# Kernel tuning notes

Hardware: AMD Instinct MI355X
Metric: run time of the kernel (lower is better)

Reference implementation:

```python
import jax, jax.numpy as jnp
import numpy as np

B, S, D, H, DH = 4, 2048, 512, 8, 64

def setup_inputs() -> dict:
    key = jax.random.key(0)
    k1, k2, k3, k4 = jax.random.split(key, 4)
    sc = 1.0 / np.sqrt(D)
    return {
        "x": jax.random.normal(k1, (B, S, D), dtype=jnp.float32),
        "Wq": jax.random.normal(k2, (H, D, DH), dtype=jnp.float32) * sc,
        "Wk": jax.random.normal(k3, (H, D, DH), dtype=jnp.float32) * sc,
        "Wv": jax.random.normal(k4, (H, D, DH), dtype=jnp.float32) * sc,
    }

def reference(x, Wq, Wk, Wv):
    # x: [B,S,D]; Wq/Wk/Wv: [H,D,DH] (stacked per-head bias-free Linear weights)
    q = jnp.einsum('bsd,hdk->bhsk', x, Wq)
    k = jnp.einsum('bsd,hdk->bhsk', x, Wk)
    v = jnp.einsum('bsd,hdk->bhsk', x, Wv)
    scale = DH ** -0.5
    scores = jax.nn.softmax(jnp.einsum('bhqk,bhsk->bhqs', q, k) * scale, axis=-1)
    out = jnp.einsum('bhqs,bhsk->bhqk', scores, v)  # [B,H,S,DH]
    # concat heads along last dim (head order matches ModuleList order)
    return out.transpose(0, 2, 1, 3).reshape(B, S, H * DH)
```

## Files before the change

### kernel.cpp

```cpp
#include <hip/hip_runtime.h>

typedef _Float16 half8  __attribute__((ext_vector_type(8)));
typedef _Float16 half4v __attribute__((ext_vector_type(4)));
typedef _Float16 half2v __attribute__((ext_vector_type(2)));
typedef __fp16   fp16x2 __attribute__((ext_vector_type(2)));
typedef float    float4v __attribute__((ext_vector_type(4)));

#define CSC 0.18033688f

__device__ __forceinline__ void async16(const _Float16* g, void* l) {
    __builtin_amdgcn_global_load_lds((const __attribute__((address_space(1))) void*)g,
                                     (__attribute__((address_space(3))) void*)l, 16, 0, 0);
}

__device__ __forceinline__ half2v pk2(float a, float b) {
    return __builtin_bit_cast(half2v, __builtin_amdgcn_cvt_pkrtz(a, b));
}

__global__ __launch_bounds__(256) void mha_prep_x(const float* __restrict__ x,
                                                  _Float16* __restrict__ xh) {
    int t = blockIdx.x * 256 + threadIdx.x;
    float4v v = ((const float4v*)x)[t];
    half4v o;
    #pragma unroll
    for (int i = 0; i < 4; ++i) o[i] = (_Float16)v[i];
    ((half4v*)xh)[t] = o;
}

__global__ __launch_bounds__(256) void mha_prep_w(const float* __restrict__ wq,
    const float* __restrict__ wk, const float* __restrict__ wv, _Float16* __restrict__ wt) {
    __shared__ __align__(16) _Float16 T[64][72];
    const int tid = threadIdx.x;
    const int blk = blockIdx.x;
    const int dt = blk & 7, h = (blk >> 3) & 7, mat = blk >> 6;
    const float* w = ((mat == 0) ? wq : (mat == 1) ? wk : wv) + h * 32768 + dt * 64 * 64;
    #pragma unroll
    for (int i = 0; i < 4; ++i) {
        int s = tid + i * 256;
        int dl = s >> 4, c4 = s & 15;
        float4v v = ((const float4v*)(w + (size_t)dl * 64))[c4];
        #pragma unroll
        for (int e = 0; e < 4; ++e) T[c4 * 4 + e][dl] = (_Float16)v[e];
    }
    __syncthreads();
    #pragma unroll
    for (int i = 0; i < 2; ++i) {
        int s = tid + i * 256;
        int dh = s >> 3, c8 = s & 7;
        half8 o;
        #pragma unroll
        for (int e = 0; e < 8; ++e) o[e] = T[dh][c8 * 8 + e];
        *(half8*)(wt + (size_t)((mat * 8 + h) * 64 + dh) * 512 + dt * 64 + c8 * 8) = o;
    }
}

__global__ __launch_bounds__(256, 3) void mha_qkv(const _Float16* __restrict__ xh,
    const _Float16* __restrict__ wt, _Float16* __restrict__ Qm, _Float16* __restrict__ Km,
    _Float16* __restrict__ Vt) {
    __shared__ __align__(16) _Float16 Ash[2][128 * 32];
    __shared__ __align__(16) _Float16 Bsh[2][128 * 32];
    const int tid = threadIdx.x;
    const int lane = tid & 63, wave = tid >> 6;
    const int quad = lane >> 4, li = lane & 15;
    const int m0 = blockIdx.x * 128, n0 = blockIdx.y * 128;
    float4v acc[4][4] = {};
    const int r0 = tid >> 2, c0 = (tid & 3) ^ ((r0 >> 1) & 3);
    const int s1 = 256 + tid, r1 = s1 >> 2, c1 = (s1 & 3) ^ ((r1 >> 1) & 3);
    const _Float16* gA0 = xh + (size_t)(m0 + r0) * 512 + c0 * 8;
    const _Float16* gA1 = xh + (size_t)(m0 + r1) * 512 + c1 * 8;
    const _Float16* gB0 = wt + (size_t)(n0 + r0) * 512 + c0 * 8;
    const _Float16* gB1 = wt + (size_t)(n0 + r1) * 512 + c1 * 8;
    const int wr = (wave >> 1) * 64, wc = (wave & 1) * 64;
    const char* aB[2]; const char* bB[2];
    #pragma unroll
    for (int bb = 0; bb < 2; ++bb) {
        aB[bb] = (const char*)Ash[bb] + (wr + li) * 64 + ((quad ^ ((li >> 1) & 3)) << 4);
        bB[bb] = (const char*)Bsh[bb] + (wc + li) * 64 + ((quad ^ ((li >> 1) & 3)) << 4);
    }
    auto stage = [&](int bb, int kk) {
        async16(gA0 + kk, (char*)Ash[bb] + wave * 1024);
        async16(gA1 + kk, (char*)Ash[bb] + 4096 + wave * 1024);
        async16(gB0 + kk, (char*)Bsh[bb] + wave * 1024);
        async16(gB1 + kk, (char*)Bsh[bb] + 4096 + wave * 1024);
    };
    auto compute = [&](int bb) {
        half8 af[4], bf[4];
        #pragma unroll
        for (int mt = 0; mt < 4; ++mt) af[mt] = *(const half8*)(aB[bb] + mt * 1024);
        #pragma unroll
        for (int nt = 0; nt < 4; ++nt) bf[nt] = *(const half8*)(bB[bb] + nt * 1024);
        #pragma unroll
        for (int mt = 0; mt < 4; ++mt)
            #pragma unroll
            for (int nt = 0; nt < 4; ++nt)
                acc[mt][nt] = __builtin_amdgcn_mfma_f32_16x16x32_f16(af[mt], bf[nt], acc[mt][nt], 0, 0, 0);
    };
    stage(0, 0);
    for (int kk = 0; kk < 512; kk += 64) {
        __syncthreads();
        stage(1, kk + 32);
        compute(0);
        __syncthreads();
        if (kk + 64 < 512) stage(0, kk + 64);
        compute(1);
    }
    const int mat = n0 >> 9;
    const float osc = (mat == 0) ? CSC : 1.0f;
    #pragma unroll
    for (int mt = 0; mt < 4; ++mt) {
        int m = m0 + wr + mt * 16 + quad * 4;
        int b = m >> 11, s = m & 2047;
        #pragma unroll
        for (int nt = 0; nt < 4; ++nt) {
            int n = n0 + wc + nt * 16 + li;
            int h = (n >> 6) & 7, dh = n & 63;
            int bh = b * 8 + h;
            if (mat == 2) {
                half4v pkv;
                #pragma unroll
                for (int r = 0; r < 4; ++r) pkv[r] = (_Float16)acc[mt][nt][r];
                *(half4v*)(Vt + ((size_t)bh * 64 + dh) * 2048 + s) = pkv;
            } else {
                _Float16* dst = (mat == 0) ? Qm : Km;
                size_t base = ((size_t)bh * 2048 + s) * 64 + dh;
                #pragma unroll
                for (int r = 0; r < 4; ++r) dst[base + (size_t)r * 64] = (_Float16)(acc[mt][nt][r] * osc);
            }
        }
    }
}

__global__ __launch_bounds__(128, 1) void mha_attn(const _Float16* __restrict__ Qm,
    const _Float16* __restrict__ Km, const _Float16* __restrict__ Vt, float* __restrict__ out) {
    __shared__ __align__(16) _Float16 KtA[2][128 * 64];
    __shared__ __align__(16) _Float16 VtA[2][64 * 128];
    const int tid = threadIdx.x, lane = tid & 63, wave = tid >> 6;
    const int quad = lane >> 4, li = lane & 15;
    const int qb = blockIdx.x, bh = blockIdx.y;
    const int b = bh >> 3, h = bh & 7;
    const _Float16* Qg = Qm + (size_t)bh * 2048 * 64;
    const _Float16* Kg = Km + (size_t)bh * 2048 * 64;
    const _Float16* Vg = Vt + (size_t)bh * 64 * 2048;
    const int q0 = qb * 128 + wave * 64;
    half8 qf[4][2];
    #pragma unroll
    for (int qt = 0; qt < 4; ++qt)
        #pragma unroll
        for (int ds = 0; ds < 2; ++ds)
            qf[qt][ds] = *(const half8*)(Qg + (size_t)(q0 + qt * 16 + li) * 64 + ds * 32 + quad * 8);
    float4v O[4][4] = {};
    float lsum[4] = {0.f, 0.f, 0.f, 0.f};
    const _Float16* pK[8]; const _Float16* pV[8];
    #pragma unroll
    for (int is = 0; is < 8; ++is) {
        int s = is * 128 + tid;
        int rk = s >> 3, sck = s & 7;
        int swk = (rk & 3) | (((rk >> 3) & 1) << 2);
        int rv = s >> 4, cv = (s & 15) ^ (rv & 15);
        pK[is] = Kg + (size_t)rk * 64 + (sck ^ swk) * 8;
        pV[is] = Vg + (size_t)rv * 2048 + cv * 8;
    }
    auto stage = [&](int bb) {
        #pragma unroll
        for (int is = 0; is < 8; ++is) {
            async16(pK[is], (char*)KtA[bb] + is * 2048 + wave * 1024);
            async16(pV[is], (char*)VtA[bb] + is * 2048 + wave * 1024);
            pK[is] += 8192;
            pV[is] += 128;
        }
    };
    const int rowE = ((li >> 2) << 3) | (li & 3);
    const int swzE = (li & 3) | (((li >> 2) & 1) << 2);
    const char *k0e[2], *k1e[2], *vBq[2];
    #pragma unroll
    for (int bb = 0; bb < 2; ++bb) {
        const char* base = (const char*)KtA[bb] + rowE * 128;
        k0e[bb] = base + ((quad ^ swzE) << 4);
        k1e[bb] = base + (((quad + 4) ^ swzE) << 4);
        vBq[bb] = (const char*)VtA[bb] + li * 256;
    }
    int coff[4];
    #pragma unroll
    for (int c = 0; c < 4; ++c) coff[c] = ((c * 4 + quad) ^ li) << 4;
    auto compute = [&](int bb) {
        #pragma unroll
        for (int c = 0; c < 4; ++c) {
            half8 f0e = *(const half8*)(k0e[bb] + c * 4096);
            half8 f1e = *(const half8*)(k1e[bb] + c * 4096);
            half8 f0o = *(const half8*)(k0e[bb] + c * 4096 + 512);
            half8 f1o = *(const half8*)(k1e[bb] + c * 4096 + 512);
            half8 pf[4];
            #pragma unroll
            for (int qt = 0; qt < 4; ++qt) {
                float4v se = {}, so = {};
                se = __builtin_amdgcn_mfma_f32_16x16x32_f16(f0e, qf[qt][0], se, 0, 0, 0);
                se = __builtin_amdgcn_mfma_f32_16x16x32_f16(f1e, qf[qt][1], se, 0, 0, 0);
                so = __builtin_amdgcn_mfma_f32_16x16x32_f16(f0o, qf[qt][0], so, 0, 0, 0);
                so = __builtin_amdgcn_mfma_f32_16x16x32_f16(f1o, qf[qt][1], so, 0, 0, 0);
                float pe[4], po[4];
                #pragma unroll
                for (int r = 0; r < 4; ++r) {
                    pe[r] = __builtin_amdgcn_exp2f(se[r]);
                    po[r] = __builtin_amdgcn_exp2f(so[r]);
                    lsum[qt] += pe[r] + po[r];
                }
                half4v a = __builtin_shufflevector(pk2(pe[0], pe[1]), pk2(pe[2], pe[3]), 0, 1, 2, 3);
                half4v o = __builtin_shufflevector(pk2(po[0], po[1]), pk2(po[2], po[3]), 0, 1, 2, 3);
                pf[qt] = __builtin_shufflevector(a, o, 0, 1, 2, 3, 4, 5, 6, 7);
            }
            #pragma unroll
            for (int dt = 0; dt < 4; ++dt) {
                half8 vf = *(const half8*)(vBq[bb] + dt * 4096 + coff[c]);
                #pragma unroll
                for (int qt = 0; qt < 4; ++qt)
                    O[qt][dt] = __builtin_amdgcn_mfma_f32_16x16x32_f16(pf[qt], vf, O[qt][dt], 0, 0, 0);
            }
        }
    };
    stage(0);
    for (int it = 0; it < 8; ++it) {
        __syncthreads();
        stage(1);
        compute(0);
        __syncthreads();
        if (it < 7) stage(0);
        compute(1);
    }
    #pragma unroll
    for (int qt = 0; qt < 4; ++qt) {
        float l = lsum[qt];
        l += __shfl_xor(l, 16);
        l += __shfl_xor(l, 32);
        #pragma unroll
        for (int r = 0; r < 4; ++r) {
            float lr = __shfl(l, quad * 4 + r);
            float inv = 1.0f / lr;
            int q = q0 + qt * 16 + quad * 4 + r;
            float* orow = out + ((size_t)(b * 2048 + q)) * 512 + h * 64;
            #pragma unroll
            for (int dt = 0; dt < 4; ++dt) orow[dt * 16 + li] = O[qt][dt][r] * inv;
        }
    }
}

extern "C" void kernel_launch(void* const* d_in, const int* in_sizes, int n_in,
                              void* d_out, int out_size, void* d_ws, size_t ws_size,
                              hipStream_t stream) {
    const float* x  = (const float*)d_in[0];
    const float* wq = (const float*)d_in[1];
    const float* wk = (const float*)d_in[2];
    const float* wv = (const float*)d_in[3];
    float* out = (float*)d_out;
    char* ws = (char*)d_ws;
    _Float16* xh = (_Float16*)(ws);
    _Float16* wt = (_Float16*)(ws + 8388608);
    _Float16* Qm = (_Float16*)(ws + 9961472);
    _Float16* Km = (_Float16*)(ws + 18350080);
    _Float16* Vt = (_Float16*)(ws + 26738688);
    if (ws_size < 35127296u) return;
    mha_prep_x<<<4096, 256, 0, stream>>>(x, xh);
    mha_prep_w<<<192, 256, 0, stream>>>(wq, wk, wv, wt);
    mha_qkv<<<dim3(64, 12), 256, 0, stream>>>(xh, wt, Qm, Km, Vt);
    mha_attn<<<dim3(16, 32), 128, 0, stream>>>(Qm, Km, Vt, out);
}
```

Before: 150.3 us.

## Split attention key range across wave pairs and merge two prep kernels

```diff
diff --git a/kernel.cpp b/kernel.cpp
--- a/kernel.cpp
+++ b/kernel.cpp
@@ -17,21 +17,21 @@
     return __builtin_bit_cast(half2v, __builtin_amdgcn_cvt_pkrtz(a, b));
 }
 
-__global__ __launch_bounds__(256) void mha_prep_x(const float* __restrict__ x,
-                                                  _Float16* __restrict__ xh) {
-    int t = blockIdx.x * 256 + threadIdx.x;
-    float4v v = ((const float4v*)x)[t];
-    half4v o;
-    #pragma unroll
-    for (int i = 0; i < 4; ++i) o[i] = (_Float16)v[i];
-    ((half4v*)xh)[t] = o;
-}
-
-__global__ __launch_bounds__(256) void mha_prep_w(const float* __restrict__ wq,
-    const float* __restrict__ wk, const float* __restrict__ wv, _Float16* __restrict__ wt) {
+__global__ __launch_bounds__(256) void mha_prep(const float* __restrict__ x,
+    const float* __restrict__ wq, const float* __restrict__ wk, const float* __restrict__ wv,
+    _Float16* __restrict__ xh, _Float16* __restrict__ wt) {
     __shared__ __align__(16) _Float16 T[64][72];
     const int tid = threadIdx.x;
-    const int blk = blockIdx.x;
+    if (blockIdx.x < 4096) {
+        int t = blockIdx.x * 256 + tid;
+        float4v v = ((const float4v*)x)[t];
+        half4v o;
+        #pragma unroll
+        for (int i = 0; i < 4; ++i) o[i] = (_Float16)v[i];
+        ((half4v*)xh)[t] = o;
+        return;
+    }
+    const int blk = blockIdx.x - 4096;
     const int dt = blk & 7, h = (blk >> 3) & 7, mat = blk >> 6;
     const float* w = ((mat == 0) ? wq : (mat == 1) ? wk : wv) + h * 32768 + dt * 64 * 64;
     #pragma unroll
@@ -130,18 +130,21 @@
     }
 }
 
-__global__ __launch_bounds__(128, 1) void mha_attn(const _Float16* __restrict__ Qm,
+__global__ __launch_bounds__(256, 2) void mha_attn(const _Float16* __restrict__ Qm,
     const _Float16* __restrict__ Km, const _Float16* __restrict__ Vt, float* __restrict__ out) {
-    __shared__ __align__(16) _Float16 KtA[2][128 * 64];
-    __shared__ __align__(16) _Float16 VtA[2][64 * 128];
+    __shared__ __align__(16) _Float16 KtA[4][64 * 64];
+    __shared__ __align__(16) _Float16 VtA[4][64 * 64];
     const int tid = threadIdx.x, lane = tid & 63, wave = tid >> 6;
     const int quad = lane >> 4, li = lane & 15;
-    const int qb = blockIdx.x, bh = blockIdx.y;
+    const int strm = wave & 1, hh = wave >> 1;
+    const int flat = blockIdx.x;
+    const int qb = (flat >> 3) & 15;
+    const int bh = ((flat >> 7) << 3) | (flat & 7);
     const int b = bh >> 3, h = bh & 7;
     const _Float16* Qg = Qm + (size_t)bh * 2048 * 64;
-    const _Float16* Kg = Km + (size_t)bh * 2048 * 64;
-    const _Float16* Vg = Vt + (size_t)bh * 64 * 2048;
-    const int q0 = qb * 128 + wave * 64;
+    const _Float16* Kg = Km + (size_t)bh * 2048 * 64 + (size_t)strm * 1024 * 64;
+    const _Float16* Vg = Vt + (size_t)bh * 64 * 2048 + (size_t)strm * 1024;
+    const int q0 = qb * 128 + hh * 64;
     half8 qf[4][2];
     #pragma unroll
     for (int qt = 0; qt < 4; ++qt)
@@ -150,23 +153,29 @@
             qf[qt][ds] = *(const half8*)(Qg + (size_t)(q0 + qt * 16 + li) * 64 + ds * 32 + quad * 8);
     float4v O[4][4] = {};
     float lsum[4] = {0.f, 0.f, 0.f, 0.f};
-    const _Float16* pK[8]; const _Float16* pV[8];
-    #pragma unroll
-    for (int is = 0; is < 8; ++is) {
-        int s = is * 128 + tid;
-        int rk = s >> 3, sck = s & 7;
+    char* Kst[2]; char* Vst[2];
+    #pragma unroll
+    for (int bb = 0; bb < 2; ++bb) {
+        Kst[bb] = (char*)KtA + (strm * 2 + bb) * 8192;
+        Vst[bb] = (char*)VtA + (strm * 2 + bb) * 8192;
+    }
+    const _Float16* pK[4]; const _Float16* pV[4];
+    #pragma unroll
+    for (int is = 0; is < 4; ++is) {
+        int c = is * 128 + hh * 64 + lane;
+        int rk = c >> 3, sck = c & 7;
         int swk = (rk & 3) | (((rk >> 3) & 1) << 2);
-        int rv = s >> 4, cv = (s & 15) ^ (rv & 15);
+        int rv = c >> 3, cv = (c & 7) ^ (rv & 7);
         pK[is] = Kg + (size_t)rk * 64 + (sck ^ swk) * 8;
         pV[is] = Vg + (size_t)rv * 2048 + cv * 8;
     }
     auto stage = [&](int bb) {
         #pragma unroll
-        for (int is = 0; is < 8; ++is) {
-            async16(pK[is], (char*)KtA[bb] + is * 2048 + wave * 1024);
-            async16(pV[is], (char*)VtA[bb] + is * 2048 + wave * 1024);
-            pK[is] += 8192;
-            pV[is] += 128;
+        for (int is = 0; is < 4; ++is) {
+            async16(pK[is], Kst[bb] + is * 2048 + hh * 1024);
+            async16(pV[is], Vst[bb] + is * 2048 + hh * 1024);
+            pK[is] += 4096;
+            pV[is] += 64;
         }
     };
     const int rowE = ((li >> 2) << 3) | (li & 3);
@@ -174,17 +183,16 @@
     const char *k0e[2], *k1e[2], *vBq[2];
     #pragma unroll
     for (int bb = 0; bb < 2; ++bb) {
-        const char* base = (const char*)KtA[bb] + rowE * 128;
-        k0e[bb] = base + ((quad ^ swzE) << 4);
-        k1e[bb] = base + (((quad + 4) ^ swzE) << 4);
-        vBq[bb] = (const char*)VtA[bb] + li * 256;
-    }
-    int coff[4];
-    #pragma unroll
-    for (int c = 0; c < 4; ++c) coff[c] = ((c * 4 + quad) ^ li) << 4;
+        k0e[bb] = Kst[bb] + rowE * 128 + ((quad ^ swzE) << 4);
+        k1e[bb] = Kst[bb] + rowE * 128 + (((quad + 4) ^ swzE) << 4);
+        vBq[bb] = Vst[bb] + li * 128;
+    }
+    int coff[2];
+    #pragma unroll
+    for (int c = 0; c < 2; ++c) coff[c] = (((c * 4 + quad) ^ (li & 7)) << 4);
     auto compute = [&](int bb) {
         #pragma unroll
-        for (int c = 0; c < 4; ++c) {
+        for (int c = 0; c < 2; ++c) {
             half8 f0e = *(const half8*)(k0e[bb] + c * 4096);
             half8 f1e = *(const half8*)(k1e[bb] + c * 4096);
             half8 f0o = *(const half8*)(k0e[bb] + c * 4096 + 512);
@@ -210,7 +218,7 @@
             }
             #pragma unroll
             for (int dt = 0; dt < 4; ++dt) {
-                half8 vf = *(const half8*)(vBq[bb] + dt * 4096 + coff[c]);
+                half8 vf = *(const half8*)(vBq[bb] + dt * 2048 + coff[c]);
                 #pragma unroll
                 for (int qt = 0; qt < 4; ++qt)
                     O[qt][dt] = __builtin_amdgcn_mfma_f32_16x16x32_f16(pf[qt], vf, O[qt][dt], 0, 0, 0);
@@ -225,6 +233,29 @@
         __syncthreads();
         if (it < 7) stage(0);
         compute(1);
+    }
+    __syncthreads();
+    float* Obuf = (float*)KtA;
+    float* Lbuf = (float*)VtA;
+    if (strm == 1) {
+        #pragma unroll
+        for (int qt = 0; qt < 4; ++qt) {
+            #pragma unroll
+            for (int dt = 0; dt < 4; ++dt)
+                ((float4v*)(Obuf + hh * 4096))[(qt * 4 + dt) * 64 + lane] = O[qt][dt];
+            Lbuf[hh * 256 + qt * 64 + lane] = lsum[qt];
+        }
+    }
+    __syncthreads();
+    if (strm == 1) return;
+    #pragma unroll
+    for (int qt = 0; qt < 4; ++qt) {
+        #pragma unroll
+        for (int dt = 0; dt < 4; ++dt) {
+            float4v o2 = ((float4v*)(Obuf + hh * 4096))[(qt * 4 + dt) * 64 + lane];
+            O[qt][dt] += o2;
+        }
+        lsum[qt] += Lbuf[hh * 256 + qt * 64 + lane];
     }
     #pragma unroll
     for (int qt = 0; qt < 4; ++qt) {
@@ -258,8 +289,7 @@
     _Float16* Km = (_Float16*)(ws + 18350080);
     _Float16* Vt = (_Float16*)(ws + 26738688);
     if (ws_size < 35127296u) return;
-    mha_prep_x<<<4096, 256, 0, stream>>>(x, xh);
-    mha_prep_w<<<192, 256, 0, stream>>>(wq, wk, wv, wt);
+    mha_prep<<<4288, 256, 0, stream>>>(x, wq, wk, wv, xh, wt);
     mha_qkv<<<dim3(64, 12), 256, 0, stream>>>(xh, wt, Qm, Km, Vt);
-    mha_attn<<<dim3(16, 32), 128, 0, stream>>>(Qm, Km, Vt, out);
-}
+    mha_attn<<<512, 256, 0, stream>>>(Qm, Km, Vt, out);
+}
```

After: 135.8 us. -9.7%, faster.
